# Optimization experiments

Measured on AMD Instinct MI355X. Metric: run time of the kernel, lower is better.

Reference implementation:

```python
import jax, jax.numpy as jnp
import numpy as np

DIM = 256
HEADS = 8
HEAD_DIM = DIM // HEADS
EDGE_TYPES = 8  # edge_type_count; table has EDGE_TYPES+1 rows, row 0 is padding
B, N = 2, 2048
EPS = 1e-5


def layer_norm(x, g, b):
    mu = jnp.mean(x, axis=-1, keepdims=True)
    var = jnp.mean(jnp.square(x - mu), axis=-1, keepdims=True)
    return (x - mu) * jax.lax.rsqrt(var + EPS) * g + b


def setup_inputs() -> dict:
    key = jax.random.key(0)
    ks = jax.random.split(key, 12)
    s = 0.02
    x = jax.random.normal(ks[0], (B, N, DIM), dtype=jnp.float32)
    edge_types = jax.random.randint(ks[1], (B, N, N), 0, EDGE_TYPES + 1, dtype=jnp.int32)
    node_mask = jax.random.randint(ks[2], (B, N), 0, 2, dtype=jnp.int32).astype(bool)
    qkv_w = jax.random.normal(ks[3], (DIM, 3 * DIM), dtype=jnp.float32) * s
    qkv_b = jnp.zeros((3 * DIM,), jnp.float32)
    proj_w = jax.random.normal(ks[4], (DIM, DIM), dtype=jnp.float32) * s
    proj_b = jnp.zeros((DIM,), jnp.float32)
    edge_bias_table = jax.random.normal(ks[5], (EDGE_TYPES + 1, HEADS), dtype=jnp.float32) * s
    edge_bias_table = edge_bias_table.at[0].set(0.0)  # padding_idx=0
    ln1_g = jnp.ones((DIM,), jnp.float32); ln1_b = jnp.zeros((DIM,), jnp.float32)
    ln2_g = jnp.ones((DIM,), jnp.float32); ln2_b = jnp.zeros((DIM,), jnp.float32)
    ffn_w1 = jax.random.normal(ks[6], (DIM, 4 * DIM), dtype=jnp.float32) * s
    ffn_b1 = jnp.zeros((4 * DIM,), jnp.float32)
    ffn_w2 = jax.random.normal(ks[7], (4 * DIM, DIM), dtype=jnp.float32) * s
    ffn_b2 = jnp.zeros((DIM,), jnp.float32)
    return dict(x=x, edge_types=edge_types, node_mask=node_mask,
                qkv_w=qkv_w, qkv_b=qkv_b, proj_w=proj_w, proj_b=proj_b,
                edge_bias_table=edge_bias_table, ln1_g=ln1_g, ln1_b=ln1_b,
                ln2_g=ln2_g, ln2_b=ln2_b, ffn_w1=ffn_w1, ffn_b1=ffn_b1,
                ffn_w2=ffn_w2, ffn_b2=ffn_b2)


def reference(x, edge_types, node_mask, qkv_w, qkv_b, proj_w, proj_b,
              edge_bias_table, ln1_g, ln1_b, ln2_g, ln2_b,
              ffn_w1, ffn_b1, ffn_w2, ffn_b2):
    scale = HEAD_DIM ** -0.5
    residual = x
    h = layer_norm(x, ln1_g, ln1_b)
    qkv = h @ qkv_w + qkv_b                         # [B,N,3*DIM]
    qkv = qkv.reshape(B, N, 3, HEADS, HEAD_DIM)
    q, k, v = (qkv[:, :, 0].transpose(0, 2, 1, 3),  # [B,H,N,d]
               qkv[:, :, 1].transpose(0, 2, 1, 3),
               qkv[:, :, 2].transpose(0, 2, 1, 3))
    scores = jnp.einsum('bhnd,bhmd->bhnm', q, k) * scale
    bias = edge_bias_table[edge_types]              # [B,N,N,H]
    scores = scores + bias.transpose(0, 3, 1, 2)    # [B,H,N,N]
    eye = jnp.eye(N, dtype=bool)
    edge_mask = (edge_types != 0) | eye[None]
    node_mask_2d = node_mask[:, None, :] & node_mask[:, :, None]
    attn_mask = edge_mask & node_mask_2d            # [B,N,N]
    scores = jnp.where(attn_mask[:, None], scores, -1e9)
    attn = jax.nn.softmax(scores, axis=-1)
    out = jnp.einsum('bhnm,bhmd->bhnd', attn, v)
    out = out.transpose(0, 2, 1, 3).reshape(B, N, DIM)
    out = (out @ proj_w + proj_b) * node_mask[:, :, None]
    x1 = residual + out
    h2 = layer_norm(x1, ln2_g, ln2_b)
    h2 = jax.nn.gelu(h2 @ ffn_w1 + ffn_b1, approximate=False) @ ffn_w2 + ffn_b2
    h2 = h2 * node_mask[:, :, None]
    return x1 + h2
```

## Files before the change

### kernel.cpp

```cpp
#include <hip/hip_runtime.h>
#include <math.h>

#define DIMM 256
#define HEADS 8
#define NB 2048
#define BB 2
#define ROWS (BB*NB)

typedef __attribute__((ext_vector_type(8))) short bf16x8;
typedef __attribute__((ext_vector_type(4))) short bf16x4;
typedef __attribute__((ext_vector_type(4))) float f32x4;

__device__ inline unsigned short f2bf(float f) {
    unsigned int u = __float_as_uint(f);
    u += 0x7FFFu + ((u >> 16) & 1u);
    return (unsigned short)(u >> 16);
}
__device__ inline float bf2f(unsigned short u) {
    return __uint_as_float(((unsigned int)u) << 16);
}

__device__ inline int get_mask(const void* nm, int fmt, int idx) {
    if (fmt) return ((const unsigned char*)nm)[idx] != 0;
    return ((const int*)nm)[idx] != 0;
}

__global__ __launch_bounds__(256) void scan_copy_kernel(
    const void* __restrict__ nmask, int* __restrict__ nv,
    unsigned short* __restrict__ qidx,
    const float* __restrict__ x, float* __restrict__ out)
{
    __shared__ int fsh;
    __shared__ int cnt[256];
    __shared__ int base[256];
    int bid = blockIdx.x, t = threadIdx.x;
    if (t == 0) fsh = 0;
    __syncthreads();
    if (((const unsigned char*)nmask)[4 * t + 1] != 0) fsh = 1;
    __syncthreads();
    int fm = fsh;
    if (bid < BB) {
        int b = bid;
        int m[8]; int c = 0;
#pragma unroll
        for (int i = 0; i < 8; ++i) {
            m[i] = get_mask(nmask, fm, b * NB + t * 8 + i);
            c += m[i];
        }
        cnt[t] = c;
        __syncthreads();
        if (t == 0) {
            int acc = 0;
            for (int i = 0; i < 256; ++i) { base[i] = acc; acc += cnt[i]; }
            nv[b] = acc;
        }
        __syncthreads();
        int off = base[t];
#pragma unroll
        for (int i = 0; i < 8; ++i) {
            int row = t * 8 + i;
            if (m[i]) qidx[b * NB + off++] = (unsigned short)row;
        }
        __syncthreads();
        if (t == 0) {
            int n = nv[b];
            unsigned short last = (n > 0) ? qidx[b * NB + n - 1] : (unsigned short)0;
            int padend = (n + 63) & ~63;
            for (int i = n; i < padend; ++i) qidx[b * NB + i] = last;
        }
    } else {
        int row = (bid - BB) * 8 + (t >> 5);
        if (!get_mask(nmask, fm, row)) {
            int c0 = (t & 31) * 8;
            float4 v0 = *(const float4*)&x[(size_t)row * DIMM + c0];
            float4 v1 = *(const float4*)&x[(size_t)row * DIMM + c0 + 4];
            *(float4*)&out[(size_t)row * DIMM + c0]     = v0;
            *(float4*)&out[(size_t)row * DIMM + c0 + 4] = v1;
        }
    }
}

__device__ inline void ln8_body(const float* __restrict__ x, const float* __restrict__ g,
                                const float* __restrict__ bb, unsigned short* __restrict__ o,
                                int xrow, int orow, int lane32) {
    int c0 = lane32 * 8;
    float4 v0 = *(const float4*)&x[(size_t)xrow * DIMM + c0];
    float4 v1 = *(const float4*)&x[(size_t)xrow * DIMM + c0 + 4];
    float s  = v0.x + v0.y + v0.z + v0.w + v1.x + v1.y + v1.z + v1.w;
    float s2 = v0.x*v0.x + v0.y*v0.y + v0.z*v0.z + v0.w*v0.w
             + v1.x*v1.x + v1.y*v1.y + v1.z*v1.z + v1.w*v1.w;
#pragma unroll
    for (int off = 16; off >= 1; off >>= 1) {
        s  += __shfl_xor(s,  off);
        s2 += __shfl_xor(s2, off);
    }
    float mean = s * (1.0f / DIMM);
    float var  = s2 * (1.0f / DIMM) - mean * mean;
    float rstd = rsqrtf(var + 1e-5f);
    float4 g0 = *(const float4*)&g[c0],  g1 = *(const float4*)&g[c0 + 4];
    float4 b0 = *(const float4*)&bb[c0], b1 = *(const float4*)&bb[c0 + 4];
    ushort4 u0, u1;
    u0.x = f2bf((v0.x - mean) * rstd * g0.x + b0.x);
    u0.y = f2bf((v0.y - mean) * rstd * g0.y + b0.y);
    u0.z = f2bf((v0.z - mean) * rstd * g0.z + b0.z);
    u0.w = f2bf((v0.w - mean) * rstd * g0.w + b0.w);
    u1.x = f2bf((v1.x - mean) * rstd * g1.x + b1.x);
    u1.y = f2bf((v1.y - mean) * rstd * g1.y + b1.y);
    u1.z = f2bf((v1.z - mean) * rstd * g1.z + b1.z);
    u1.w = f2bf((v1.w - mean) * rstd * g1.w + b1.w);
    *(ushort4*)&o[(size_t)orow * DIMM + c0]     = u0;
    *(ushort4*)&o[(size_t)orow * DIMM + c0 + 4] = u1;
}

__global__ __launch_bounds__(256) void prep_kernel(
    const float* __restrict__ w0, const float* __restrict__ w1,
    const float* __restrict__ w2, const float* __restrict__ w3,
    unsigned short* __restrict__ o0, unsigned short* __restrict__ o1,
    unsigned short* __restrict__ o2, unsigned short* __restrict__ o3,
    const float* __restrict__ x, const float* __restrict__ ln1_g,
    const float* __restrict__ ln1_b, unsigned short* __restrict__ h_ln,
    const int* __restrict__ etypes,
    unsigned char* __restrict__ emaskP,
    const int* __restrict__ nv, const unsigned short* __restrict__ qidx)
{
    __shared__ float tile[64][65];
    int bid = blockIdx.x, t = threadIdx.x;
    if (bid < 192) {
        const float* src; unsigned short* dst; int K, N, idx;
        if (bid < 48)       { src = w0; dst = o0; K = 256;  N = 768;  idx = bid; }
        else if (bid < 64)  { src = w1; dst = o1; K = 256;  N = 256;  idx = bid - 48; }
        else if (bid < 128) { src = w2; dst = o2; K = 256;  N = 1024; idx = bid - 64; }
        else                { src = w3; dst = o3; K = 1024; N = 256;  idx = bid - 128; }
        int ntiles = N >> 6;
        int k0 = (idx / ntiles) * 64, n0 = (idx % ntiles) * 64;
        int r = t >> 4, c4 = (t & 15) * 4;
#pragma unroll
        for (int i = 0; i < 4; ++i) {
            float4 v = *(const float4*)&src[(size_t)(k0 + r + i * 16) * N + n0 + c4];
            tile[r + i * 16][c4 + 0] = v.x;
            tile[r + i * 16][c4 + 1] = v.y;
            tile[r + i * 16][c4 + 2] = v.z;
            tile[r + i * 16][c4 + 3] = v.w;
        }
        __syncthreads();
#pragma unroll
        for (int i = 0; i < 4; ++i) {
            int n = n0 + r + i * 16;
            ushort4 u;
            u.x = f2bf(tile[c4 + 0][r + i * 16]);
            u.y = f2bf(tile[c4 + 1][r + i * 16]);
            u.z = f2bf(tile[c4 + 2][r + i * 16]);
            u.w = f2bf(tile[c4 + 3][r + i * 16]);
            *(ushort4*)&dst[(size_t)n * K + k0 + c4] = u;
        }
    } else if (bid < 704) {
        int slotg = (bid - 192) * 8 + (t >> 5);
        int b = slotg >> 11, sl = slotg & 2047;
        int nvp = (nv[b] + 63) & ~63;
        if (sl < nvp) {
            int row = qidx[b * NB + sl];
            ln8_body(x, ln1_g, ln1_b, h_ln, b * NB + row, slotg, t & 31);
        }
    } else {
        int unit = (bid - 704) * 4 + (t >> 6);
        int lane = t & 63, quad = lane >> 4, l15 = lane & 15;
        int b = unit >> 12;
        int qt16 = (unit >> 5) & 127;
        int kt = unit & 31;
        int nvb = nv[b];
        int nvp = (nvb + 63) & ~63;
        if (qt16 * 16 >= nvb || kt * 64 >= nvp) return;
        int slot = qt16 * 16 + l15;
        int validq = slot < nvb;
        int qr = qidx[b * NB + slot];
        const int* erow = etypes + (size_t)(b * NB + qr) * NB;
        unsigned int dw[2] = {0u, 0u};
#pragma unroll
        for (int t16 = 0; t16 < 4; ++t16) {
#pragma unroll
            for (int r = 0; r < 4; ++r) {
                int ks = kt * 64 + t16 * 16 + quad * 4 + r;
                unsigned int code = 0u;
                if (validq && ks < nvb) {
                    int korig = qidx[b * NB + ks];
                    int et = erow[korig];
                    if ((et != 0) || (korig == qr)) code = (unsigned int)(et + 1);
                }
                dw[t16 >> 1] |= code << ((t16 & 1) * 16 + r * 4);
            }
        }
        int2 o = {(int)dw[0], (int)dw[1]};
        *(int2*)(emaskP + (size_t)unit * 512 + lane * 8) = o;
    }
}

__global__ __launch_bounds__(256) void gemm_qkv_mfma(
    const unsigned short* __restrict__ A, const unsigned short* __restrict__ Bt,
    const float* __restrict__ bias, const int* __restrict__ nv,
    unsigned short* __restrict__ qkvh, unsigned short* __restrict__ vT)
{
    const int K = 256;
    int t = threadIdx.x, w = t >> 6, l = t & 63;
    int l15 = l & 15, quad = l >> 4;
    int n0 = blockIdx.x * 64;
    int m0c = blockIdx.y * 64;
    int b = blockIdx.z;
    int nvp = (nv[b] + 63) & ~63;
    if (m0c >= nvp) return;
    const unsigned short* ap = A + (size_t)(b * NB + m0c + w * 16 + l15) * K + quad * 8;
    const unsigned short* bp = Bt + (size_t)(n0 + l15) * K + quad * 8;

    f32x4 acc[4];
#pragma unroll
    for (int c = 0; c < 4; ++c) acc[c] = (f32x4){0.f, 0.f, 0.f, 0.f};

    bf16x8 aA, bA[4], aB, bB[4];
    auto ld = [&](bf16x8& af, bf16x8 (&bf)[4], int k0) {
        af = *(const bf16x8*)(ap + k0);
#pragma unroll
        for (int c = 0; c < 4; ++c)
            bf[c] = *(const bf16x8*)(bp + (size_t)(c * 16) * K + k0);
    };
    auto pr = [&](const bf16x8& af, const bf16x8 (&bf)[4]) {
#pragma unroll
        for (int c = 0; c < 4; ++c)
            acc[c] = __builtin_amdgcn_mfma_f32_16x16x32_bf16(af, bf[c], acc[c], 0, 0, 0);
    };
    ld(aA, bA, 0);
    for (int k0 = 0; k0 < K; k0 += 64) {
        ld(aB, bB, k0 + 32);
        pr(aA, bA);
        if (k0 + 64 < K) ld(aA, bA, k0 + 64);
        pr(aB, bB);
    }

    if (n0 < 512) {
        float sc = (n0 < 256) ? 0.17677669529663689f : 1.0f;
#pragma unroll
        for (int r = 0; r < 4; ++r) {
            int slot = b * NB + m0c + w * 16 + quad * 4 + r;
#pragma unroll
            for (int c = 0; c < 4; ++c) {
                int col = n0 + c * 16 + l15;
                qkvh[(size_t)slot * 512 + col] = f2bf((acc[c][r] + bias[col]) * sc);
            }
        }
    } else {
        int n = m0c + w * 16 + quad * 4;
#pragma unroll
        for (int c = 0; c < 4; ++c) {
            int col = n0 + c * 16 + l15 - 512;
            int hidx = col >> 5, d = col & 31;
            float bs = bias[n0 + c * 16 + l15];
            ushort4 u;
            u.x = f2bf(acc[c][0] + bs);
            u.y = f2bf(acc[c][1] + bs);
            u.z = f2bf(acc[c][2] + bs);
            u.w = f2bf(acc[c][3] + bs);
            *(ushort4*)&vT[(size_t)((b * HEADS + hidx) * 32 + d) * NB + n] = u;
        }
    }
}

__global__ __launch_bounds__(256) void attn_mfma(
    const unsigned short* __restrict__ qkvh,
    const unsigned short* __restrict__ vT,
    const unsigned char* __restrict__ emaskP,
    const float* __restrict__ table,
    const int* __restrict__ nv,
    unsigned short* __restrict__ OpH, float* __restrict__ lpart)
{
    __shared__ unsigned short P[4][16][72];
    __shared__ float tab2m[16];

    int t = threadIdx.x;
    int w = t >> 6, l = t & 63;
    int l15 = l & 15, quad = l >> 4;
    int h = blockIdx.x;
    int qt = blockIdx.y;
    int z = blockIdx.z, b = z >> 2, sp = z & 3;

    if (t < 16) tab2m[t] = (t >= 1 && t < 10) ? __expf(table[(t - 1) * 8 + h]) : 0.f;
    __syncthreads();

    int nvb = nv[b];
    int qt16 = qt * 4 + w;
    int q0c = qt16 * 16;
    if (q0c >= nvb) return;

    int nkt = (nvb + 63) >> 6;
    int tps = (nkt + 3) >> 2;
    int kbase = sp * tps * 64;
    int kend = min(kbase + tps * 64, nkt * 64);

    bf16x8 bq = *(const bf16x8*)(qkvh + (size_t)(b * NB + q0c + l15) * 512 + h * 32 + quad * 8);

    const unsigned short* kp = qkvh + (size_t)(b * NB + l15) * 512 + 256 + h * 32 + quad * 8;
    const unsigned short* vp = vT + (size_t)((b * HEADS + h) * 32 + l15) * NB + quad * 8;
    const unsigned char* ep = emaskP + (size_t)((b * 128 + qt16) * 32) * 512 + l * 8;

    float lacc = 0.f;
    f32x4 O0 = {0.f, 0.f, 0.f, 0.f}, O1 = {0.f, 0.f, 0.f, 0.f};

    bf16x8 kA[4], kB[4];
    bf16x8 vA[2][2], vB[2][2];
    int2 eA, eB;

    auto loadtile = [&](bf16x8 (&kf)[4], bf16x8 (&vf)[2][2], int2& ef, int m0) {
#pragma unroll
        for (int t16 = 0; t16 < 4; ++t16)
            kf[t16] = *(const bf16x8*)(kp + (size_t)(m0 + t16 * 16) * 512);
#pragma unroll
        for (int ks = 0; ks < 2; ++ks) {
            vf[ks][0] = *(const bf16x8*)(vp + m0 + ks * 32);
            vf[ks][1] = *(const bf16x8*)(vp + 16 * NB + m0 + ks * 32);
        }
        ef = *(const int2*)(ep + (size_t)(m0 >> 6) * 512);
    };

    auto process = [&](const bf16x8 (&kf)[4], const bf16x8 (&vf)[2][2], const int2& ef) {
#pragma unroll
        for (int t16 = 0; t16 < 4; ++t16) {
            f32x4 zero = {0.f, 0.f, 0.f, 0.f};
            f32x4 sT = __builtin_amdgcn_mfma_f32_16x16x32_bf16(kf[t16], bq, zero, 0, 0, 0);
            unsigned int e = ((unsigned int)((t16 < 2) ? ef.x : ef.y)) >> ((t16 & 1) * 16);
            float p0 = __expf(sT[0]) * tab2m[e & 0xFu];
            float p1 = __expf(sT[1]) * tab2m[(e >> 4) & 0xFu];
            float p2 = __expf(sT[2]) * tab2m[(e >> 8) & 0xFu];
            float p3 = __expf(sT[3]) * tab2m[(e >> 12) & 0xFu];
            lacc += (p0 + p1) + (p2 + p3);
            bf16x4 pb;
            pb[0] = (short)f2bf(p0); pb[1] = (short)f2bf(p1);
            pb[2] = (short)f2bf(p2); pb[3] = (short)f2bf(p3);
            *(bf16x4*)&P[w][l15][t16 * 16 + quad * 4] = pb;
        }
#pragma unroll
        for (int ks = 0; ks < 2; ++ks) {
            bf16x8 pa = *(const bf16x8*)&P[w][l15][ks * 32 + quad * 8];
            O0 = __builtin_amdgcn_mfma_f32_16x16x32_bf16(pa, vf[ks][0], O0, 0, 0, 0);
            O1 = __builtin_amdgcn_mfma_f32_16x16x32_bf16(pa, vf[ks][1], O1, 0, 0, 0);
        }
    };

    if (kbase < kend) {
        loadtile(kA, vA, eA, kbase);
        for (int m0 = kbase; m0 < kend; m0 += 128) {
            int n1 = (m0 + 64 < kend) ? m0 + 64 : kbase;
            loadtile(kB, vB, eB, n1);
            process(kA, vA, eA);
            if (m0 + 128 < kend) loadtile(kA, vA, eA, m0 + 128);
            if (m0 + 64 < kend) process(kB, vB, eB);
        }
    }

    lacc += __shfl_xor(lacc, 16);
    lacc += __shfl_xor(lacc, 32);

    unsigned short* Ob = OpH + (size_t)sp * ROWS * DIMM;
#pragma unroll
    for (int r = 0; r < 4; ++r) {
        int slot = q0c + quad * 4 + r;
        if (slot < nvb) {
            Ob[(size_t)(b * NB + slot) * DIMM + h * 32 + l15]      = f2bf(O0[r]);
            Ob[(size_t)(b * NB + slot) * DIMM + h * 32 + 16 + l15] = f2bf(O1[r]);
        }
    }
    if (quad == 0 && q0c + l15 < nvb)
        lpart[(size_t)sp * ROWS * 8 + (size_t)(b * NB + q0c + l15) * 8 + h] = lacc;
}

__global__ __launch_bounds__(1024) void megaback(
    const unsigned short* __restrict__ OpH, const float* __restrict__ lpart,
    const unsigned short* __restrict__ projT, const float* __restrict__ proj_b,
    const float* __restrict__ x,
    const float* __restrict__ g2, const float* __restrict__ b2,
    const unsigned short* __restrict__ f1T, const float* __restrict__ ffn_b1,
    const unsigned short* __restrict__ f2T, const float* __restrict__ ffn_b2,
    const int* __restrict__ nv, const unsigned short* __restrict__ qidx,
    float* __restrict__ out)
{
    __shared__ float rinv_l[16][8];
    __shared__ float stats[16][2];
    __shared__ float redn[16][16][2];
    __shared__ unsigned short Astage[16][264];
    __shared__ float x1s[16][260];
    __shared__ unsigned short hstage[16][264];
    __shared__ unsigned short midstage[16][1032];

    int t = threadIdx.x;
    int w = t >> 6, l = t & 63;
    int l15 = l & 15, quad = l >> 4;
    int b = blockIdx.x >> 7;
    int s0 = (blockIdx.x & 127) * 16;
    int nvb = nv[b];
    if (s0 >= nvb) return;
    int slot0 = b * NB + s0;

    if (t < 128) {
        int row = t >> 3, h = t & 7;
        float s = 0.f;
#pragma unroll
        for (int sp = 0; sp < 4; ++sp)
            s += lpart[(size_t)sp * ROWS * 8 + (size_t)(slot0 + row) * 8 + h];
        rinv_l[row][h] = (s > 0.f) ? 1.f / s : 0.f;
    }
    __syncthreads();

    {
        int row = t >> 6, col4 = (t & 63) * 4;
        float rinv = rinv_l[row][col4 >> 5];
        float o0 = 0.f, o1 = 0.f, o2 = 0.f, o3 = 0.f;
#pragma unroll
        for (int sp = 0; sp < 4; ++sp) {
            ushort4 u = *(const ushort4*)&OpH[(size_t)sp * ROWS * DIMM +
                                             (size_t)(slot0 + row) * DIMM + col4];
            o0 += bf2f(u.x); o1 += bf2f(u.y); o2 += bf2f(u.z); o3 += bf2f(u.w);
        }
        ushort4 u;
        u.x = f2bf(o0 * rinv); u.y = f2bf(o1 * rinv);
        u.z = f2bf(o2 * rinv); u.w = f2bf(o3 * rinv);
        *(ushort4*)&Astage[row][col4] = u;
    }
    __syncthreads();

    {
        int col = w * 16 + l15;
        f32x4 acc = (f32x4){0.f, 0.f, 0.f, 0.f};
        const unsigned short* bp = projT + (size_t)col * 256 + quad * 8;
        bf16x8 sb[4];
#pragma unroll
        for (int i = 0; i < 4; ++i) sb[i] = *(const bf16x8*)(bp + i * 32);
#pragma unroll
        for (int ch = 0; ch < 8; ++ch) {
            bf16x8 a = *(const bf16x8*)&Astage[l15][ch * 32 + quad * 8];
            acc = __builtin_amdgcn_mfma_f32_16x16x32_bf16(a, sb[ch & 3], acc, 0, 0, 0);
            if (ch + 4 < 8) sb[ch & 3] = *(const bf16x8*)(bp + (ch + 4) * 32);
        }
        float bs = proj_b[col];
#pragma unroll
        for (int r = 0; r < 4; ++r) {
            int row = quad * 4 + r;
            int grow = b * NB + qidx[(size_t)slot0 + row - (size_t)b * NB + b * NB];
            grow = b * NB + qidx[(size_t)(slot0 + row)];
            float v = (acc[r] + bs) + x[(size_t)grow * DIMM + col];
            x1s[row][col] = v;
            float s = v, s2 = v * v;
#pragma unroll
            for (int off = 1; off < 16; off <<= 1) {
                s += __shfl_xor(s, off); s2 += __shfl_xor(s2, off);
            }
            if (l15 == 0) { redn[row][w][0] = s; redn[row][w][1] = s2; }
        }
    }
    __syncthreads();
    if (t < 16) {
        float s = 0.f, s2 = 0.f;
#pragma unroll
        for (int ww = 0; ww < 16; ++ww) { s += redn[t][ww][0]; s2 += redn[t][ww][1]; }
        float mean = s * (1.f / DIMM);
        float var  = s2 * (1.f / DIMM) - mean * mean;
        stats[t][0] = mean; stats[t][1] = rsqrtf(var + 1e-5f);
    }
    __syncthreads();

    {
        int col = w * 16 + l15;
        float gv = g2[col], bv = b2[col];
#pragma unroll
        for (int r = 0; r < 4; ++r) {
            int row = quad * 4 + r;
            float hv = (x1s[row][col] - stats[row][0]) * stats[row][1] * gv + bv;
            hstage[row][col] = f2bf(hv);
        }
    }
    __syncthreads();

    {
        f32x4 acc[4];
#pragma unroll
        for (int c = 0; c < 4; ++c) acc[c] = (f32x4){0.f, 0.f, 0.f, 0.f};
        const unsigned short* bp = f1T + (size_t)(w * 64 + l15) * 256 + quad * 8;
        bf16x8 bA[4], bB[4];
#pragma unroll
        for (int c = 0; c < 4; ++c) bA[c] = *(const bf16x8*)(bp + (size_t)(c * 16) * 256);
#pragma unroll
        for (int ch = 0; ch < 8; ++ch) {
            bf16x8 a = *(const bf16x8*)&hstage[l15][ch * 32 + quad * 8];
            if (ch + 1 < 8) {
#pragma unroll
                for (int c = 0; c < 4; ++c)
                    bB[c] = *(const bf16x8*)(bp + (size_t)(c * 16) * 256 + (ch + 1) * 32);
            }
#pragma unroll
            for (int c = 0; c < 4; ++c)
                acc[c] = __builtin_amdgcn_mfma_f32_16x16x32_bf16(a, bA[c], acc[c], 0, 0, 0);
#pragma unroll
            for (int c = 0; c < 4; ++c) bA[c] = bB[c];
        }
#pragma unroll
        for (int c = 0; c < 4; ++c) {
            int col = w * 64 + c * 16 + l15;
            float bs = ffn_b1[col];
#pragma unroll
            for (int r = 0; r < 4; ++r) {
                float v = acc[c][r] + bs;
                float x2 = v * v;
                float p = v * fmaf(0.07135481f, x2, 1.5957691f);
                float e = __expf(p);
                float gl = v * (e / (e + 1.f));
                midstage[quad * 4 + r][col] = f2bf(gl);
            }
        }
    }
    __syncthreads();

    {
        int col = w * 16 + l15;
        f32x4 acc = (f32x4){0.f, 0.f, 0.f, 0.f};
        const unsigned short* bp = f2T + (size_t)col * 1024 + quad * 8;
        bf16x8 sb[4];
#pragma unroll
        for (int i = 0; i < 4; ++i) sb[i] = *(const bf16x8*)(bp + i * 32);
#pragma unroll
        for (int ch = 0; ch < 32; ++ch) {
            bf16x8 a = *(const bf16x8*)&midstage[l15][ch * 32 + quad * 8];
            acc = __builtin_amdgcn_mfma_f32_16x16x32_bf16(a, sb[ch & 3], acc, 0, 0, 0);
            if (ch + 4 < 32) sb[ch & 3] = *(const bf16x8*)(bp + (ch + 4) * 32);
        }
        float bs = ffn_b2[col];
#pragma unroll
        for (int r = 0; r < 4; ++r) {
            int row = quad * 4 + r;
            if (s0 + row < nvb) {
                int grow = b * NB + qidx[(size_t)(slot0 + row)];
                out[(size_t)grow * DIMM + col] = x1s[row][col] + (acc[r] + bs);
            }
        }
    }
}

extern "C" void kernel_launch(void* const* d_in, const int* in_sizes, int n_in,
                              void* d_out, int out_size, void* d_ws, size_t ws_size,
                              hipStream_t stream) {
    const float* x       = (const float*)d_in[0];
    const int*   etypes  = (const int*)d_in[1];
    const void*  nmask   = d_in[2];
    const float* qkv_w   = (const float*)d_in[3];
    const float* qkv_b   = (const float*)d_in[4];
    const float* proj_w  = (const float*)d_in[5];
    const float* proj_b  = (const float*)d_in[6];
    const float* table   = (const float*)d_in[7];
    const float* ln1_g   = (const float*)d_in[8];
    const float* ln1_b   = (const float*)d_in[9];
    const float* ln2_g   = (const float*)d_in[10];
    const float* ln2_b   = (const float*)d_in[11];
    const float* ffn_w1  = (const float*)d_in[12];
    const float* ffn_b1  = (const float*)d_in[13];
    const float* ffn_w2  = (const float*)d_in[14];
    const float* ffn_b2  = (const float*)d_in[15];
    float* out = (float*)d_out;
    float* ws  = (float*)d_ws;

    float* lpart = ws;
    unsigned short* ub = (unsigned short*)(ws + 131072);
    unsigned short* h_ln   = ub;
    unsigned short* qkvh   = ub + 1048576;
    unsigned short* vT     = ub + 3145728;
    unsigned short* OpH    = ub + 4194304;
    unsigned short* qkvT   = ub + 8388608;
    unsigned short* projT  = ub + 8585216;
    unsigned short* f1T    = ub + 8650752;
    unsigned short* f2T    = ub + 8912896;
    unsigned char* emaskP  = (unsigned char*)(ub + 9175040);
    unsigned short* qidx   = ub + 11272192;
    int* nv                = (int*)(ub + 11276288);

    scan_copy_kernel<<<dim3(BB + ROWS/8), dim3(256), 0, stream>>>(nmask, nv, qidx, x, out);
    prep_kernel<<<dim3(2752), dim3(256), 0, stream>>>(
        qkv_w, proj_w, ffn_w1, ffn_w2, qkvT, projT, f1T, f2T,
        x, ln1_g, ln1_b, h_ln, etypes, emaskP, nv, qidx);
    gemm_qkv_mfma<<<dim3(12, 32, BB), dim3(256), 0, stream>>>(h_ln, qkvT, qkv_b, nv, qkvh, vT);
    attn_mfma<<<dim3(HEADS, NB/64, BB*4), dim3(256), 0, stream>>>(
        qkvh, vT, emaskP, table, nv, OpH, lpart);
    megaback<<<dim3(2 * 128), dim3(1024), 0, stream>>>(
        OpH, lpart, projT, proj_b, x, ln2_g, ln2_b,
        f1T, ffn_b1, f2T, ffn_b2, nv, qidx, out);
}
```

Before: 203.5 us.

## Rebalance prologue kernels and halve megaback row tile to raise block count

```diff
diff --git a/kernel.cpp b/kernel.cpp
--- a/kernel.cpp
+++ b/kernel.cpp
@@ -25,21 +25,25 @@
     return ((const int*)nm)[idx] != 0;
 }
 
-__global__ __launch_bounds__(256) void scan_copy_kernel(
+__global__ __launch_bounds__(256) void scan_w2bft_kernel(
     const void* __restrict__ nmask, int* __restrict__ nv,
     unsigned short* __restrict__ qidx,
-    const float* __restrict__ x, float* __restrict__ out)
+    const float* __restrict__ w0, const float* __restrict__ w1,
+    const float* __restrict__ w2, const float* __restrict__ w3,
+    unsigned short* __restrict__ o0, unsigned short* __restrict__ o1,
+    unsigned short* __restrict__ o2, unsigned short* __restrict__ o3)
 {
+    __shared__ float tile[64][65];
     __shared__ int fsh;
     __shared__ int cnt[256];
     __shared__ int base[256];
     int bid = blockIdx.x, t = threadIdx.x;
-    if (t == 0) fsh = 0;
-    __syncthreads();
-    if (((const unsigned char*)nmask)[4 * t + 1] != 0) fsh = 1;
-    __syncthreads();
-    int fm = fsh;
     if (bid < BB) {
+        if (t == 0) fsh = 0;
+        __syncthreads();
+        if (((const unsigned char*)nmask)[4 * t + 1] != 0) fsh = 1;
+        __syncthreads();
+        int fm = fsh;
         int b = bid;
         int m[8]; int c = 0;
 #pragma unroll
@@ -69,13 +73,33 @@
             for (int i = n; i < padend; ++i) qidx[b * NB + i] = last;
         }
     } else {
-        int row = (bid - BB) * 8 + (t >> 5);
-        if (!get_mask(nmask, fm, row)) {
-            int c0 = (t & 31) * 8;
-            float4 v0 = *(const float4*)&x[(size_t)row * DIMM + c0];
-            float4 v1 = *(const float4*)&x[(size_t)row * DIMM + c0 + 4];
-            *(float4*)&out[(size_t)row * DIMM + c0]     = v0;
-            *(float4*)&out[(size_t)row * DIMM + c0 + 4] = v1;
+        int wb = bid - BB;
+        const float* src; unsigned short* dst; int K, N, idx;
+        if (wb < 48)       { src = w0; dst = o0; K = 256;  N = 768;  idx = wb; }
+        else if (wb < 64)  { src = w1; dst = o1; K = 256;  N = 256;  idx = wb - 48; }
+        else if (wb < 128) { src = w2; dst = o2; K = 256;  N = 1024; idx = wb - 64; }
+        else               { src = w3; dst = o3; K = 1024; N = 256;  idx = wb - 128; }
+        int ntiles = N >> 6;
+        int k0 = (idx / ntiles) * 64, n0 = (idx % ntiles) * 64;
+        int r = t >> 4, c4 = (t & 15) * 4;
+#pragma unroll
+        for (int i = 0; i < 4; ++i) {
+            float4 v = *(const float4*)&src[(size_t)(k0 + r + i * 16) * N + n0 + c4];
+            tile[r + i * 16][c4 + 0] = v.x;
+            tile[r + i * 16][c4 + 1] = v.y;
+            tile[r + i * 16][c4 + 2] = v.z;
+            tile[r + i * 16][c4 + 3] = v.w;
+        }
+        __syncthreads();
+#pragma unroll
+        for (int i = 0; i < 4; ++i) {
+            int n = n0 + r + i * 16;
+            ushort4 u;
+            u.x = f2bf(tile[c4 + 0][r + i * 16]);
+            u.y = f2bf(tile[c4 + 1][r + i * 16]);
+            u.z = f2bf(tile[c4 + 2][r + i * 16]);
+            u.w = f2bf(tile[c4 + 3][r + i * 16]);
+            *(ushort4*)&dst[(size_t)n * K + k0 + c4] = u;
         }
     }
 }
@@ -113,48 +137,15 @@
 }
 
 __global__ __launch_bounds__(256) void prep_kernel(
-    const float* __restrict__ w0, const float* __restrict__ w1,
-    const float* __restrict__ w2, const float* __restrict__ w3,
-    unsigned short* __restrict__ o0, unsigned short* __restrict__ o1,
-    unsigned short* __restrict__ o2, unsigned short* __restrict__ o3,
     const float* __restrict__ x, const float* __restrict__ ln1_g,
     const float* __restrict__ ln1_b, unsigned short* __restrict__ h_ln,
     const int* __restrict__ etypes,
     unsigned char* __restrict__ emaskP,
     const int* __restrict__ nv, const unsigned short* __restrict__ qidx)
 {
-    __shared__ float tile[64][65];
     int bid = blockIdx.x, t = threadIdx.x;
-    if (bid < 192) {
-        const float* src; unsigned short* dst; int K, N, idx;
-        if (bid < 48)       { src = w0; dst = o0; K = 256;  N = 768;  idx = bid; }
-        else if (bid < 64)  { src = w1; dst = o1; K = 256;  N = 256;  idx = bid - 48; }
-        else if (bid < 128) { src = w2; dst = o2; K = 256;  N = 1024; idx = bid - 64; }
-        else                { src = w3; dst = o3; K = 1024; N = 256;  idx = bid - 128; }
-        int ntiles = N >> 6;
-        int k0 = (idx / ntiles) * 64, n0 = (idx % ntiles) * 64;
-        int r = t >> 4, c4 = (t & 15) * 4;
-#pragma unroll
-        for (int i = 0; i < 4; ++i) {
-            float4 v = *(const float4*)&src[(size_t)(k0 + r + i * 16) * N + n0 + c4];
-            tile[r + i * 16][c4 + 0] = v.x;
-            tile[r + i * 16][c4 + 1] = v.y;
-            tile[r + i * 16][c4 + 2] = v.z;
-            tile[r + i * 16][c4 + 3] = v.w;
-        }
-        __syncthreads();
-#pragma unroll
-        for (int i = 0; i < 4; ++i) {
-            int n = n0 + r + i * 16;
-            ushort4 u;
-            u.x = f2bf(tile[c4 + 0][r + i * 16]);
-            u.y = f2bf(tile[c4 + 1][r + i * 16]);
-            u.z = f2bf(tile[c4 + 2][r + i * 16]);
-            u.w = f2bf(tile[c4 + 3][r + i * 16]);
-            *(ushort4*)&dst[(size_t)n * K + k0 + c4] = u;
-        }
-    } else if (bid < 704) {
-        int slotg = (bid - 192) * 8 + (t >> 5);
+    if (bid < 512) {
+        int slotg = bid * 8 + (t >> 5);
         int b = slotg >> 11, sl = slotg & 2047;
         int nvp = (nv[b] + 63) & ~63;
         if (sl < nvp) {
@@ -162,7 +153,7 @@
             ln8_body(x, ln1_g, ln1_b, h_ln, b * NB + row, slotg, t & 31);
         }
     } else {
-        int unit = (bid - 704) * 4 + (t >> 6);
+        int unit = (bid - 512) * 4 + (t >> 6);
         int lane = t & 63, quad = lane >> 4, l15 = lane & 15;
         int b = unit >> 12;
         int qt16 = (unit >> 5) & 127;
@@ -372,31 +363,51 @@
 __global__ __launch_bounds__(1024) void megaback(
     const unsigned short* __restrict__ OpH, const float* __restrict__ lpart,
     const unsigned short* __restrict__ projT, const float* __restrict__ proj_b,
-    const float* __restrict__ x,
+    const float* __restrict__ x, const void* __restrict__ nmask,
     const float* __restrict__ g2, const float* __restrict__ b2,
     const unsigned short* __restrict__ f1T, const float* __restrict__ ffn_b1,
     const unsigned short* __restrict__ f2T, const float* __restrict__ ffn_b2,
     const int* __restrict__ nv, const unsigned short* __restrict__ qidx,
     float* __restrict__ out)
 {
-    __shared__ float rinv_l[16][8];
-    __shared__ float stats[16][2];
-    __shared__ float redn[16][16][2];
-    __shared__ unsigned short Astage[16][264];
-    __shared__ float x1s[16][260];
-    __shared__ unsigned short hstage[16][264];
-    __shared__ unsigned short midstage[16][1032];
+    __shared__ float rinv_l[8][8];
+    __shared__ float stats[8][2];
+    __shared__ float redn[8][16][2];
+    __shared__ unsigned short Astage[8][264];
+    __shared__ float x1s[8][260];
+    __shared__ unsigned short hstage[8][264];
+    __shared__ unsigned short midstage[8][1032];
+    __shared__ int fsh;
 
     int t = threadIdx.x;
+    int bid = blockIdx.x;
+
+    if (bid >= 512) {
+        if (t == 0) fsh = 0;
+        __syncthreads();
+        if (((const unsigned char*)nmask)[4 * t + 1] != 0) fsh = 1;
+        __syncthreads();
+        int fm = fsh;
+        int row = (bid - 512) * 32 + (t >> 5);
+        if (!get_mask(nmask, fm, row)) {
+            int c0 = (t & 31) * 8;
+            float4 v0 = *(const float4*)&x[(size_t)row * DIMM + c0];
+            float4 v1 = *(const float4*)&x[(size_t)row * DIMM + c0 + 4];
+            *(float4*)&out[(size_t)row * DIMM + c0]     = v0;
+            *(float4*)&out[(size_t)row * DIMM + c0 + 4] = v1;
+        }
+        return;
+    }
+
     int w = t >> 6, l = t & 63;
     int l15 = l & 15, quad = l >> 4;
-    int b = blockIdx.x >> 7;
-    int s0 = (blockIdx.x & 127) * 16;
+    int b = bid >> 8;
+    int s0 = (bid & 255) * 8;
     int nvb = nv[b];
     if (s0 >= nvb) return;
     int slot0 = b * NB + s0;
 
-    if (t < 128) {
+    if (t < 64) {
         int row = t >> 3, h = t & 7;
         float s = 0.f;
 #pragma unroll
@@ -406,7 +417,7 @@
     }
     __syncthreads();
 
-    {
+    if (t < 512) {
         int row = t >> 6, col4 = (t & 63) * 4;
         float rinv = rinv_l[row][col4 >> 5];
         float o0 = 0.f, o1 = 0.f, o2 = 0.f, o3 = 0.f;
@@ -432,28 +443,29 @@
         for (int i = 0; i < 4; ++i) sb[i] = *(const bf16x8*)(bp + i * 32);
 #pragma unroll
         for (int ch = 0; ch < 8; ++ch) {
-            bf16x8 a = *(const bf16x8*)&Astage[l15][ch * 32 + quad * 8];
+            bf16x8 a = *(const bf16x8*)&Astage[l15 & 7][ch * 32 + quad * 8];
             acc = __builtin_amdgcn_mfma_f32_16x16x32_bf16(a, sb[ch & 3], acc, 0, 0, 0);
             if (ch + 4 < 8) sb[ch & 3] = *(const bf16x8*)(bp + (ch + 4) * 32);
         }
         float bs = proj_b[col];
 #pragma unroll
         for (int r = 0; r < 4; ++r) {
-            int row = quad * 4 + r;
-            int grow = b * NB + qidx[(size_t)slot0 + row - (size_t)b * NB + b * NB];
-            grow = b * NB + qidx[(size_t)(slot0 + row)];
-            float v = (acc[r] + bs) + x[(size_t)grow * DIMM + col];
-            x1s[row][col] = v;
-            float s = v, s2 = v * v;
-#pragma unroll
-            for (int off = 1; off < 16; off <<= 1) {
-                s += __shfl_xor(s, off); s2 += __shfl_xor(s2, off);
+            int row16 = quad * 4 + r;
+            if (row16 < 8) {
+                int grow = b * NB + qidx[(size_t)(slot0 + row16)];
+                float v = (acc[r] + bs) + x[(size_t)grow * DIMM + col];
+                x1s[row16][col] = v;
+                float s = v, s2 = v * v;
+#pragma unroll
+                for (int off = 1; off < 16; off <<= 1) {
+                    s += __shfl_xor(s, off); s2 += __shfl_xor(s2, off);
+                }
+                if (l15 == 0) { redn[row16][w][0] = s; redn[row16][w][1] = s2; }
             }
-            if (l15 == 0) { redn[row][w][0] = s; redn[row][w][1] = s2; }
         }
     }
     __syncthreads();
-    if (t < 16) {
+    if (t < 8) {
         float s = 0.f, s2 = 0.f;
 #pragma unroll
         for (int ww = 0; ww < 16; ++ww) { s += redn[t][ww][0]; s2 += redn[t][ww][1]; }
@@ -468,9 +480,11 @@
         float gv = g2[col], bv = b2[col];
 #pragma unroll
         for (int r = 0; r < 4; ++r) {
-            int row = quad * 4 + r;
-            float hv = (x1s[row][col] - stats[row][0]) * stats[row][1] * gv + bv;
-            hstage[row][col] = f2bf(hv);
+            int row16 = quad * 4 + r;
+            if (row16 < 8) {
+                float hv = (x1s[row16][col] - stats[row16][0]) * stats[row16][1] * gv + bv;
+                hstage[row16][col] = f2bf(hv);
+            }
         }
     }
     __syncthreads();
@@ -485,7 +499,7 @@
         for (int c = 0; c < 4; ++c) bA[c] = *(const bf16x8*)(bp + (size_t)(c * 16) * 256);
 #pragma unroll
         for (int ch = 0; ch < 8; ++ch) {
-            bf16x8 a = *(const bf16x8*)&hstage[l15][ch * 32 + quad * 8];
+            bf16x8 a = *(const bf16x8*)&hstage[l15 & 7][ch * 32 + quad * 8];
             if (ch + 1 < 8) {
 #pragma unroll
                 for (int c = 0; c < 4; ++c)
@@ -503,12 +517,15 @@
             float bs = ffn_b1[col];
 #pragma unroll
             for (int r = 0; r < 4; ++r) {
-                float v = acc[c][r] + bs;
-                float x2 = v * v;
-                float p = v * fmaf(0.07135481f, x2, 1.5957691f);
-                float e = __expf(p);
-                float gl = v * (e / (e + 1.f));
-                midstage[quad * 4 + r][col] = f2bf(gl);
+                int row16 = quad * 4 + r;
+                if (row16 < 8) {
+                    float v = acc[c][r] + bs;
+                    float x2 = v * v;
+                    float p = v * fmaf(0.07135481f, x2, 1.5957691f);
+                    float e = __expf(p);
+                    float gl = v * (e / (e + 1.f));
+                    midstage[row16][col] = f2bf(gl);
+                }
             }
         }
     }
@@ -523,17 +540,17 @@
         for (int i = 0; i < 4; ++i) sb[i] = *(const bf16x8*)(bp + i * 32);
 #pragma unroll
         for (int ch = 0; ch < 32; ++ch) {
-            bf16x8 a = *(const bf16x8*)&midstage[l15][ch * 32 + quad * 8];
+            bf16x8 a = *(const bf16x8*)&midstage[l15 & 7][ch * 32 + quad * 8];
             acc = __builtin_amdgcn_mfma_f32_16x16x32_bf16(a, sb[ch & 3], acc, 0, 0, 0);
             if (ch + 4 < 32) sb[ch & 3] = *(const bf16x8*)(bp + (ch + 4) * 32);
         }
         float bs = ffn_b2[col];
 #pragma unroll
         for (int r = 0; r < 4; ++r) {
-            int row = quad * 4 + r;
-            if (s0 + row < nvb) {
-                int grow = b * NB + qidx[(size_t)(slot0 + row)];
-                out[(size_t)grow * DIMM + col] = x1s[row][col] + (acc[r] + bs);
+            int row16 = quad * 4 + r;
+            if (row16 < 8 && s0 + row16 < nvb) {
+                int grow = b * NB + qidx[(size_t)(slot0 + row16)];
+                out[(size_t)grow * DIMM + col] = x1s[row16][col] + (acc[r] + bs);
             }
         }
     }
@@ -575,14 +592,14 @@
     unsigned short* qidx   = ub + 11272192;
     int* nv                = (int*)(ub + 11276288);
 
-    scan_copy_kernel<<<dim3(BB + ROWS/8), dim3(256), 0, stream>>>(nmask, nv, qidx, x, out);
-    prep_kernel<<<dim3(2752), dim3(256), 0, stream>>>(
-        qkv_w, proj_w, ffn_w1, ffn_w2, qkvT, projT, f1T, f2T,
+    scan_w2bft_kernel<<<dim3(BB + 192), dim3(256), 0, stream>>>(
+        nmask, nv, qidx, qkv_w, proj_w, ffn_w1, ffn_w2, qkvT, projT, f1T, f2T);
+    prep_kernel<<<dim3(2560), dim3(256), 0, stream>>>(
         x, ln1_g, ln1_b, h_ln, etypes, emaskP, nv, qidx);
     gemm_qkv_mfma<<<dim3(12, 32, BB), dim3(256), 0, stream>>>(h_ln, qkvT, qkv_b, nv, qkvh, vT);
     attn_mfma<<<dim3(HEADS, NB/64, BB*4), dim3(256), 0, stream>>>(
         qkvh, vT, emaskP, table, nv, OpH, lpart);
-    megaback<<<dim3(2 * 128), dim3(1024), 0, stream>>>(
-        OpH, lpart, projT, proj_b, x, ln2_g, ln2_b,
+    megaback<<<dim3(512 + ROWS/32), dim3(1024), 0, stream>>>(
+        OpH, lpart, projT, proj_b, x, nmask, ln2_g, ln2_b,
         f1T, ffn_b1, f2T, ffn_b2, nv, qidx, out);
 }
```

Result: slower. 231.2 us (+13.6%).
